# Kernel tuning notes

Measured on AMD Instinct MI355X. Metric: run time of the kernel, lower is better.

Reference implementation:

```python
import jax, jax.numpy as jnp
import numpy as np


def setup_inputs() -> dict:
    key = jax.random.key(0)
    k1, k2, k3, k4 = jax.random.split(key, 4)
    T, B, D, S = 4096, 16, 128, 256
    inputs = jax.random.normal(k1, (T, B, D), dtype=jnp.float32)
    z0 = jnp.zeros((B, S), dtype=jnp.float32)
    # parameters, initialized as in the torch module
    log_neg_a = jnp.full((S,), -0.5, dtype=jnp.float32)
    b = jax.random.normal(k2, (S, D), dtype=jnp.float32) * 0.01
    log_dt = jnp.log(jnp.full((S,), 0.05, dtype=jnp.float32))
    return {"inputs": inputs, "z0": z0, "log_neg_a": log_neg_a, "b": b, "log_dt": log_dt}


def reference(inputs, z0, log_neg_a, b, log_dt):
    # discretized diagonal SSM parameters
    a_real = -jnp.exp(jnp.clip(log_neg_a, -8.0, 4.0))            # [S]
    dt = jnp.exp(jnp.clip(log_dt, -8.0, 1.0))                    # [S]
    a_bar = jnp.exp(dt * a_real)                                 # [S]
    x = dt * a_real
    ratio = jnp.where(jnp.abs(x) < 1e-6, dt, jnp.expm1(x) / a_real)
    b_bar = ratio[:, None] * b                                   # [S, D]

    # precompute input projection for all timesteps: [T, B, S]
    ub = jnp.einsum('tbd,sd->tbs', inputs, b_bar)

    def step(z, u_t):
        z = a_bar[None, :] * z + u_t                             # [B, S]
        return z, z

    _, outs = jax.lax.scan(step, z0, ub)                          # [T, B, S]
    return outs
```

## Files before the change

kernel.cpp:

```cpp
#include <hip/hip_runtime.h>
#include <hip/hip_bf16.h>

#define T_  4096
#define B_  16
#define D_  128
#define S_  256
#define WND 64
#define C4  (T_/WND)

using bf8   = __attribute__((ext_vector_type(8))) short;
using f32x4 = __attribute__((ext_vector_type(4))) float;

__device__ inline float bfbits(unsigned short h) {
    return __builtin_bit_cast(float, (unsigned)h << 16);
}
__device__ inline unsigned short bf16bits(float f) {
    return __hip_bfloat16_raw(__float2bfloat16(f)).x;
}

__global__ __launch_bounds__(256) void k_params(
        const float* __restrict__ lna, const float* __restrict__ bmat,
        const float* __restrict__ ldt,
        float* __restrict__ abar, float* __restrict__ a64,
        __hip_bfloat16* __restrict__ bbar) {
    if (blockIdx.x < 128) {
        int idx = blockIdx.x * 256 + threadIdx.x;
        int s = idx >> 7;
        float la = fminf(fmaxf(lna[s], -8.f), 4.f);
        float ar = -expf(la);
        float lt = fminf(fmaxf(ldt[s], -8.f), 1.f);
        float dt = expf(lt);
        float xx = dt * ar;
        float ratio = (fabsf(xx) < 1e-6f) ? dt : (expm1f(xx) / ar);
        bbar[idx] = __float2bfloat16(ratio * bmat[idx]);
    } else {
        int s = threadIdx.x;
        float la = fminf(fmaxf(lna[s], -8.f), 4.f);
        float ar = -expf(la);
        float lt = fminf(fmaxf(ldt[s], -8.f), 1.f);
        float dt = expf(lt);
        float ab = expf(dt * ar);
        abar[s] = ab;
        float p = ab;
#pragma unroll
        for (int j = 0; j < 6; ++j) p *= p;
        a64[s] = p;
    }
}

__global__ __launch_bounds__(256, 4) void k_gemm(
        const float* __restrict__ x, const __hip_bfloat16* __restrict__ bbar,
        const float* __restrict__ abar,
        __hip_bfloat16* __restrict__ ub, float* __restrict__ e64) {
    const int c = blockIdx.x, b = blockIdx.y;
    __shared__ char LDS[WND * 512];
    const int tid = threadIdx.x, lane = tid & 63, w = tid >> 6;
    const int l15 = lane & 15, l4 = lane >> 4;

#pragma unroll
    for (int k = 0; k < 8; ++k) {
        int idx = tid + k * 256;
        int row = idx >> 5, seg = idx & 31;
        float4 v = *(const float4*)(x + ((size_t)(c * WND + row) * B_ + b) * D_ + seg * 4);
        __hip_bfloat162 lo = __float22bfloat162_rn(make_float2(v.x, v.y));
        __hip_bfloat162 hi = __float22bfloat162_rn(make_float2(v.z, v.w));
        uint2 pk = { *(unsigned*)&lo, *(unsigned*)&hi };
        int off = (row * 256 + seg * 8) ^ ((row & 7) << 4);
        *(uint2*)(LDS + off) = pk;
    }
    __syncthreads();

    f32x4 acc[4][4] = {};
    for (int j = 0; j < 4; ++j) {
        bf8 bfrag[4];
        int s = w * 64 + j * 16 + l15;
#pragma unroll
        for (int kk = 0; kk < 4; ++kk)
            bfrag[kk] = *(const bf8*)((const short*)bbar + s * D_ + kk * 32 + l4 * 8);
#pragma unroll
        for (int i = 0; i < 4; ++i) {
            bf8 af[4];
            int tr = i * 16 + l15;
#pragma unroll
            for (int kk = 0; kk < 4; ++kk) {
                int off = (tr * 256 + kk * 64 + l4 * 16) ^ ((tr & 7) << 4);
                af[kk] = *(const bf8*)(LDS + off);
            }
#pragma unroll
            for (int kk = 0; kk < 4; ++kk)
                acc[i][j] = __builtin_amdgcn_mfma_f32_16x16x32_bf16(
                                af[kk], bfrag[kk], acc[i][j], 0, 0, 0);
        }
    }
    __syncthreads();

#pragma unroll
    for (int j = 0; j < 4; ++j) {
        int s = w * 64 + j * 16 + l15;
        float a  = abar[s];
        float a2 = a * a, a4 = a2 * a2, a8 = a4 * a4, a16 = a8 * a8;
        float lf = (l4 == 0) ? a8 * a4 : (l4 == 1) ? a8 : (l4 == 2) ? a4 : 1.f;
        float e = 0.f;
#pragma unroll
        for (int i = 0; i < 4; ++i) {
            unsigned short h0 = bf16bits(acc[i][j][0]);
            unsigned short h1 = bf16bits(acc[i][j][1]);
            unsigned short h2 = bf16bits(acc[i][j][2]);
            unsigned short h3 = bf16bits(acc[i][j][3]);
            float inner = bfbits(h0);
            inner = fmaf(inner, a, bfbits(h1));
            inner = fmaf(inner, a, bfbits(h2));
            inner = fmaf(inner, a, bfbits(h3));
            e = fmaf(e, a16, inner);
            int row0 = i * 16 + l4 * 4;
            *(unsigned short*)(LDS + (((row0    ) * 512 + s * 2) ^ (l4 << 5))) = h0;
            *(unsigned short*)(LDS + (((row0 + 1) * 512 + s * 2) ^ (l4 << 5))) = h1;
            *(unsigned short*)(LDS + (((row0 + 2) * 512 + s * 2) ^ (l4 << 5))) = h2;
            *(unsigned short*)(LDS + (((row0 + 3) * 512 + s * 2) ^ (l4 << 5))) = h3;
        }
        e *= lf;
        e += __shfl_xor(e, 16);
        e += __shfl_xor(e, 32);
        if (l4 == 0) e64[((size_t)c * B_ + b) * S_ + s] = e;
    }
    __syncthreads();

    char* op = (char*)(ub + ((size_t)b * T_ + c * WND) * S_);
#pragma unroll
    for (int k = 0; k < 8; ++k) {
        int o = k * 4096 + tid * 16;
        int swz = (2 * k + (w >> 1)) & 3;
        uint4 v = *(uint4*)(LDS + (o ^ (swz << 5)));
        *(uint4*)(op + o) = v;
    }
}

__global__ __launch_bounds__(256) void k_carry(
        const float* __restrict__ e64, const float* __restrict__ a64,
        const float* __restrict__ z0, float* __restrict__ cin) {
    const int b = blockIdx.x, s = threadIdx.x;
    float ev[C4];
#pragma unroll
    for (int c = 0; c < C4; ++c)
        ev[c] = e64[((size_t)c * B_ + b) * S_ + s];
    float aw = a64[s];
    float Z = z0[b * S_ + s];
#pragma unroll
    for (int c = 0; c < C4; ++c) {
        cin[((size_t)c * B_ + b) * S_ + s] = Z;
        Z = fmaf(aw, Z, ev[c]);
    }
}

__global__ __launch_bounds__(256) void k_scan(
        const __hip_bfloat16* __restrict__ ub, const float* __restrict__ cin,
        const float* __restrict__ abar, float* __restrict__ out) {
    const int c = blockIdx.x, g = blockIdx.y;
    const int w = threadIdx.x >> 6, lane = threadIdx.x & 63;
    const int b = g * 2 + (w >> 1);
    const int s0 = (w & 1) * 128 + lane * 2;
    float2 a = *(const float2*)(abar + s0);
    float2 z = *(const float2*)(cin + ((size_t)c * B_ + b) * S_ + s0);
    const char* up = (const char*)(ub + ((size_t)b * T_ + c * WND) * S_ + s0);
    float* op = out + ((size_t)(c * WND) * B_ + b) * S_ + s0;
#pragma unroll 8
    for (int t = 0; t < WND; ++t) {
        ushort2 v = *(const ushort2*)up;
        z.x = fmaf(a.x, z.x, bfbits(v.x));
        z.y = fmaf(a.y, z.y, bfbits(v.y));
        *(float2*)op = z;
        up += S_ * 2;
        op += (size_t)B_ * S_;
    }
}

extern "C" void kernel_launch(void* const* d_in, const int* in_sizes, int n_in,
                              void* d_out, int out_size, void* d_ws, size_t ws_size,
                              hipStream_t stream) {
    const float* x   = (const float*)d_in[0];
    const float* z0  = (const float*)d_in[1];
    const float* lna = (const float*)d_in[2];
    const float* bm  = (const float*)d_in[3];
    const float* ldt = (const float*)d_in[4];
    float* out = (float*)d_out;

    char* ws = (char*)d_ws;
    float*          abar = (float*)ws;
    float*          a64  = (float*)(ws + 4096);
    __hip_bfloat16* bbar = (__hip_bfloat16*)(ws + 8192);
    float*          e64  = (float*)(ws + (128 << 10));
    float*          cin  = (float*)(ws + (128 << 10) + (1 << 20));
    __hip_bfloat16* ub   = (__hip_bfloat16*)(ws + (4 << 20));

    k_params<<<129, 256, 0, stream>>>(lna, bm, ldt, abar, a64, bbar);
    k_gemm<<<dim3(C4, B_), 256, 0, stream>>>(x, bbar, abar, ub, e64);
    k_carry<<<B_, 256, 0, stream>>>(e64, a64, z0, cin);
    k_scan<<<dim3(C4, B_/2), 256, 0, stream>>>(ub, cin, abar, out);
}
```

Baseline: 48.57 us.

## Halve scan window and fold carry propagation into scan kernel

```diff
diff --git a/kernel.cpp b/kernel.cpp
--- a/kernel.cpp
+++ b/kernel.cpp
@@ -5,7 +5,7 @@
 #define B_  16
 #define D_  128
 #define S_  256
-#define WND 64
+#define WND 32
 #define C4  (T_/WND)
 
 using bf8   = __attribute__((ext_vector_type(8))) short;
@@ -21,7 +21,7 @@
 __global__ __launch_bounds__(256) void k_params(
         const float* __restrict__ lna, const float* __restrict__ bmat,
         const float* __restrict__ ldt,
-        float* __restrict__ abar, float* __restrict__ a64,
+        float* __restrict__ abar, float* __restrict__ aw32,
         __hip_bfloat16* __restrict__ bbar) {
     if (blockIdx.x < 128) {
         int idx = blockIdx.x * 256 + threadIdx.x;
@@ -43,22 +43,22 @@
         abar[s] = ab;
         float p = ab;
 #pragma unroll
-        for (int j = 0; j < 6; ++j) p *= p;
-        a64[s] = p;
-    }
-}
-
-__global__ __launch_bounds__(256, 4) void k_gemm(
+        for (int j = 0; j < 5; ++j) p *= p;
+        aw32[s] = p;
+    }
+}
+
+__global__ __launch_bounds__(256, 6) void k_gemm(
         const float* __restrict__ x, const __hip_bfloat16* __restrict__ bbar,
         const float* __restrict__ abar,
-        __hip_bfloat16* __restrict__ ub, float* __restrict__ e64) {
+        __hip_bfloat16* __restrict__ ub, float* __restrict__ e32) {
     const int c = blockIdx.x, b = blockIdx.y;
     __shared__ char LDS[WND * 512];
     const int tid = threadIdx.x, lane = tid & 63, w = tid >> 6;
     const int l15 = lane & 15, l4 = lane >> 4;
 
 #pragma unroll
-    for (int k = 0; k < 8; ++k) {
+    for (int k = 0; k < 4; ++k) {
         int idx = tid + k * 256;
         int row = idx >> 5, seg = idx & 31;
         float4 v = *(const float4*)(x + ((size_t)(c * WND + row) * B_ + b) * D_ + seg * 4);
@@ -70,7 +70,7 @@
     }
     __syncthreads();
 
-    f32x4 acc[4][4] = {};
+    f32x4 acc[2][4] = {};
     for (int j = 0; j < 4; ++j) {
         bf8 bfrag[4];
         int s = w * 64 + j * 16 + l15;
@@ -78,7 +78,7 @@
         for (int kk = 0; kk < 4; ++kk)
             bfrag[kk] = *(const bf8*)((const short*)bbar + s * D_ + kk * 32 + l4 * 8);
 #pragma unroll
-        for (int i = 0; i < 4; ++i) {
+        for (int i = 0; i < 2; ++i) {
             bf8 af[4];
             int tr = i * 16 + l15;
 #pragma unroll
@@ -102,7 +102,7 @@
         float lf = (l4 == 0) ? a8 * a4 : (l4 == 1) ? a8 : (l4 == 2) ? a4 : 1.f;
         float e = 0.f;
 #pragma unroll
-        for (int i = 0; i < 4; ++i) {
+        for (int i = 0; i < 2; ++i) {
             unsigned short h0 = bf16bits(acc[i][j][0]);
             unsigned short h1 = bf16bits(acc[i][j][1]);
             unsigned short h2 = bf16bits(acc[i][j][2]);
@@ -121,13 +121,13 @@
         e *= lf;
         e += __shfl_xor(e, 16);
         e += __shfl_xor(e, 32);
-        if (l4 == 0) e64[((size_t)c * B_ + b) * S_ + s] = e;
+        if (l4 == 0) e32[((size_t)c * B_ + b) * S_ + s] = e;
     }
     __syncthreads();
 
     char* op = (char*)(ub + ((size_t)b * T_ + c * WND) * S_);
 #pragma unroll
-    for (int k = 0; k < 8; ++k) {
+    for (int k = 0; k < 4; ++k) {
         int o = k * 4096 + tid * 16;
         int swz = (2 * k + (w >> 1)) & 3;
         uint4 v = *(uint4*)(LDS + (o ^ (swz << 5)));
@@ -135,32 +135,35 @@
     }
 }
 
-__global__ __launch_bounds__(256) void k_carry(
-        const float* __restrict__ e64, const float* __restrict__ a64,
-        const float* __restrict__ z0, float* __restrict__ cin) {
-    const int b = blockIdx.x, s = threadIdx.x;
-    float ev[C4];
-#pragma unroll
-    for (int c = 0; c < C4; ++c)
-        ev[c] = e64[((size_t)c * B_ + b) * S_ + s];
-    float aw = a64[s];
-    float Z = z0[b * S_ + s];
-#pragma unroll
-    for (int c = 0; c < C4; ++c) {
-        cin[((size_t)c * B_ + b) * S_ + s] = Z;
-        Z = fmaf(aw, Z, ev[c]);
-    }
-}
-
 __global__ __launch_bounds__(256) void k_scan(
-        const __hip_bfloat16* __restrict__ ub, const float* __restrict__ cin,
-        const float* __restrict__ abar, float* __restrict__ out) {
+        const __hip_bfloat16* __restrict__ ub, const float* __restrict__ e32,
+        const float* __restrict__ abar, const float* __restrict__ aw32,
+        const float* __restrict__ z0, float* __restrict__ out) {
     const int c = blockIdx.x, g = blockIdx.y;
     const int w = threadIdx.x >> 6, lane = threadIdx.x & 63;
     const int b = g * 2 + (w >> 1);
     const int s0 = (w & 1) * 128 + lane * 2;
-    float2 a = *(const float2*)(abar + s0);
-    float2 z = *(const float2*)(cin + ((size_t)c * B_ + b) * S_ + s0);
+
+    float2 a  = *(const float2*)(abar + s0);
+    float2 aw = *(const float2*)(aw32 + s0);
+    float2 z  = *(const float2*)(z0 + b * S_ + s0);
+
+#pragma unroll
+    for (int cp0 = 0; cp0 < C4; cp0 += 16) {
+        float2 ev[16];
+#pragma unroll
+        for (int k = 0; k < 16; ++k)
+            ev[k] = *(const float2*)(e32 + ((size_t)(cp0 + k) * B_ + b) * S_ + s0);
+#pragma unroll
+        for (int k = 0; k < 16; ++k) {
+            float zx = fmaf(aw.x, z.x, ev[k].x);
+            float zy = fmaf(aw.y, z.y, ev[k].y);
+            bool p = (cp0 + k) < c;
+            z.x = p ? zx : z.x;
+            z.y = p ? zy : z.y;
+        }
+    }
+
     const char* up = (const char*)(ub + ((size_t)b * T_ + c * WND) * S_ + s0);
     float* op = out + ((size_t)(c * WND) * B_ + b) * S_ + s0;
 #pragma unroll 8
@@ -186,14 +189,12 @@
 
     char* ws = (char*)d_ws;
     float*          abar = (float*)ws;
-    float*          a64  = (float*)(ws + 4096);
+    float*          aw32 = (float*)(ws + 4096);
     __hip_bfloat16* bbar = (__hip_bfloat16*)(ws + 8192);
-    float*          e64  = (float*)(ws + (128 << 10));
-    float*          cin  = (float*)(ws + (128 << 10) + (1 << 20));
+    float*          e32  = (float*)(ws + (128 << 10));
     __hip_bfloat16* ub   = (__hip_bfloat16*)(ws + (4 << 20));
 
-    k_params<<<129, 256, 0, stream>>>(lna, bm, ldt, abar, a64, bbar);
-    k_gemm<<<dim3(C4, B_), 256, 0, stream>>>(x, bbar, abar, ub, e64);
-    k_carry<<<B_, 256, 0, stream>>>(e64, a64, z0, cin);
-    k_scan<<<dim3(C4, B_/2), 256, 0, stream>>>(ub, cin, abar, out);
-}
+    k_params<<<129, 256, 0, stream>>>(lna, bm, ldt, abar, aw32, bbar);
+    k_gemm<<<dim3(C4, B_), 256, 0, stream>>>(x, bbar, abar, ub, e32);
+    k_scan<<<dim3(C4, B_/2), 256, 0, stream>>>(ub, e32, abar, aw32, z0, out);
+}
```

Measured after the change: 69.19 us. 1.42x slower.

## Fuse carry propagation into scan kernel by recomputing window carries per block

Applied to the files above, without the earlier changes.

```diff
diff --git a/kernel.cpp b/kernel.cpp
--- a/kernel.cpp
+++ b/kernel.cpp
@@ -48,7 +48,7 @@
     }
 }
 
-__global__ __launch_bounds__(256, 4) void k_gemm(
+__global__ __launch_bounds__(256, 5) void k_gemm(
         const float* __restrict__ x, const __hip_bfloat16* __restrict__ bbar,
         const float* __restrict__ abar,
         __hip_bfloat16* __restrict__ ub, float* __restrict__ e64) {
@@ -135,32 +135,35 @@
     }
 }
 
-__global__ __launch_bounds__(256) void k_carry(
-        const float* __restrict__ e64, const float* __restrict__ a64,
-        const float* __restrict__ z0, float* __restrict__ cin) {
-    const int b = blockIdx.x, s = threadIdx.x;
-    float ev[C4];
-#pragma unroll
-    for (int c = 0; c < C4; ++c)
-        ev[c] = e64[((size_t)c * B_ + b) * S_ + s];
-    float aw = a64[s];
-    float Z = z0[b * S_ + s];
-#pragma unroll
-    for (int c = 0; c < C4; ++c) {
-        cin[((size_t)c * B_ + b) * S_ + s] = Z;
-        Z = fmaf(aw, Z, ev[c]);
-    }
-}
-
 __global__ __launch_bounds__(256) void k_scan(
-        const __hip_bfloat16* __restrict__ ub, const float* __restrict__ cin,
-        const float* __restrict__ abar, float* __restrict__ out) {
+        const __hip_bfloat16* __restrict__ ub, const float* __restrict__ e64,
+        const float* __restrict__ abar, const float* __restrict__ a64,
+        const float* __restrict__ z0, float* __restrict__ out) {
     const int c = blockIdx.x, g = blockIdx.y;
     const int w = threadIdx.x >> 6, lane = threadIdx.x & 63;
     const int b = g * 2 + (w >> 1);
     const int s0 = (w & 1) * 128 + lane * 2;
-    float2 a = *(const float2*)(abar + s0);
-    float2 z = *(const float2*)(cin + ((size_t)c * B_ + b) * S_ + s0);
+
+    float2 a  = *(const float2*)(abar + s0);
+    float2 aw = *(const float2*)(a64 + s0);
+    float2 z  = *(const float2*)(z0 + b * S_ + s0);
+
+#pragma unroll
+    for (int cp0 = 0; cp0 < C4; cp0 += 16) {
+        float2 ev[16];
+#pragma unroll
+        for (int k = 0; k < 16; ++k)
+            ev[k] = *(const float2*)(e64 + ((size_t)(cp0 + k) * B_ + b) * S_ + s0);
+#pragma unroll
+        for (int k = 0; k < 16; ++k) {
+            float zx = fmaf(aw.x, z.x, ev[k].x);
+            float zy = fmaf(aw.y, z.y, ev[k].y);
+            bool p = (cp0 + k) < c;
+            z.x = p ? zx : z.x;
+            z.y = p ? zy : z.y;
+        }
+    }
+
     const char* up = (const char*)(ub + ((size_t)b * T_ + c * WND) * S_ + s0);
     float* op = out + ((size_t)(c * WND) * B_ + b) * S_ + s0;
 #pragma unroll 8
@@ -189,11 +192,9 @@
     float*          a64  = (float*)(ws + 4096);
     __hip_bfloat16* bbar = (__hip_bfloat16*)(ws + 8192);
     float*          e64  = (float*)(ws + (128 << 10));
-    float*          cin  = (float*)(ws + (128 << 10) + (1 << 20));
     __hip_bfloat16* ub   = (__hip_bfloat16*)(ws + (4 << 20));
 
     k_params<<<129, 256, 0, stream>>>(lna, bm, ldt, abar, a64, bbar);
     k_gemm<<<dim3(C4, B_), 256, 0, stream>>>(x, bbar, abar, ub, e64);
-    k_carry<<<B_, 256, 0, stream>>>(e64, a64, z0, cin);
-    k_scan<<<dim3(C4, B_/2), 256, 0, stream>>>(ub, cin, abar, out);
-}
+    k_scan<<<dim3(C4, B_ / 2), 256, 0, stream>>>(ub, e64, abar, a64, z0, out);
+}
```

Result: slower. 52.65 us (+8.4%).
